# Kernel tuning notes

Hardware: AMD Instinct MI355X
Metric: run time of the kernel (lower is better)

Reference implementation:

```python
import jax, jax.numpy as jnp
import numpy as np

T, D = 10240, 64          # rows of base tensor, head dim (orig: 5, 4)
L = T // 5                # ragged split unit (orig split offsets 2/5 and 1/5)
SCALE = 1.0 / np.sqrt(D).astype(np.float32)


def setup_inputs() -> dict:
    key = jax.random.key(0)
    base_tensor = jax.random.normal(key, (T, D), dtype=jnp.float32)
    return {"base_tensor": base_tensor}


def _sdpa(q, k, v):
    # single-head SDPA over one ragged segment: q:(Sq,D) k,v:(Skv,D)
    scores = jnp.einsum('qd,kd->qk', q, k) * SCALE
    probs = jax.nn.softmax(scores, axis=-1)
    return jnp.einsum('qk,kd->qd', probs, v)


def reference(base_tensor):
    t1 = base_tensor                      # (T, D), orig view(5,4)
    t2 = t1 * 10.0
    # query path is detached in the original (clone().detach().requires_grad_())
    t1q = jax.lax.stop_gradient(t1)
    # ragged segments: q = [t1[:2L], t1[2L:]], kv = [t2[:L], t2[L:]]
    out0 = _sdpa(t1q[: 2 * L], t2[:L], t2[:L])
    out1 = _sdpa(t1q[2 * L :], t2[L:], t2[L:])
    loss = out0.sum() + out1.sum()        # sum over nested tensor values
    return loss
```

## Files before the change

kernel.cpp:

```cpp
#include <hip/hip_runtime.h>
#include <math.h>


#define T_ROWS 10240
#define SCALE2   1.80336880f
#define INV_S2   0.55451774f
#define SKIP_THR 35.0f

typedef __bf16 bf16x8 __attribute__((ext_vector_type(8)));
typedef float  f32x16 __attribute__((ext_vector_type(16)));
typedef float  f32x4v __attribute__((ext_vector_type(4)));

__device__ __forceinline__ float ex2(float x) {
    return __builtin_amdgcn_exp2f(x);
}

__device__ __forceinline__ float max16(const f32x16& a) {
    float h0 = fmaxf(fmaxf(a[0],  a[1]),  fmaxf(a[2],  a[3]));
    float h1 = fmaxf(fmaxf(a[4],  a[5]),  fmaxf(a[6],  a[7]));
    float h2 = fmaxf(fmaxf(a[8],  a[9]),  fmaxf(a[10], a[11]));
    float h3 = fmaxf(fmaxf(a[12], a[13]), fmaxf(a[14], a[15]));
    return fmaxf(fmaxf(h0, h1), fmaxf(h2, h3));
}

__global__ __launch_bounds__(256)
void prep_kernel(const float* __restrict__ base, __bf16* __restrict__ khi,
                 __bf16* __restrict__ klo, float* __restrict__ w,
                 float* __restrict__ selfs, float* __restrict__ Znm,
                 float* __restrict__ out) {
    int tid = threadIdx.x;
    if (blockIdx.x == 0 && tid == 0) *out = 0.f;
    if (tid < 64) Znm[blockIdx.x * 64 + tid] = 0.f;

    int row = blockIdx.x * 32 + (tid >> 3);
    int c0  = (tid & 7) << 3;
    const float* p = base + (size_t)row * 64 + c0;
    f32x4v a = *(const f32x4v*)p;
    f32x4v b = *(const f32x4v*)(p + 4);

    float sum = ((a[0] + a[1]) + (a[2] + a[3])) + ((b[0] + b[1]) + (b[2] + b[3]));
    float sq = a[0] * a[0];
    sq = fmaf(a[1], a[1], sq); sq = fmaf(a[2], a[2], sq); sq = fmaf(a[3], a[3], sq);
    sq = fmaf(b[0], b[0], sq); sq = fmaf(b[1], b[1], sq);
    sq = fmaf(b[2], b[2], sq); sq = fmaf(b[3], b[3], sq);
    #pragma unroll
    for (int off = 1; off < 8; off <<= 1) {
        sum += __shfl_xor(sum, off);
        sq  += __shfl_xor(sq, off);
    }
    if ((tid & 7) == 0) { w[row] = 10.0f * sum; selfs[row] = SCALE2 * sq; }

    bf16x8 h, l;
    #pragma unroll
    for (int j = 0; j < 4; ++j) {
        __bf16 h0 = (__bf16)a[j];
        h[j] = h0; l[j] = (__bf16)(a[j] - (float)h0);
        __bf16 h1 = (__bf16)b[j];
        h[j + 4] = h1; l[j + 4] = (__bf16)(b[j] - (float)h1);
    }
    int kt = row >> 5, lr = row & 31;
    int st = c0 >> 4, lh = (c0 >> 3) & 1;
    size_t dst = (size_t)kt * 2048 + st * 512 + lh * 256 + lr * 8;
    *(bf16x8*)(khi + dst) = h;
    *(bf16x8*)(klo + dst) = l;
}

__global__ __launch_bounds__(256, 4)
void attn_kernel(const __bf16* __restrict__ khi, const __bf16* __restrict__ klo,
                 const float* __restrict__ w, const float* __restrict__ selfs,
                 float* __restrict__ Znm) {
    const int lane  = threadIdx.x & 63;
    const int l31   = lane & 31;
    const int lhalf = lane >> 5;
    const int wv    = blockIdx.x * 4 + (threadIdx.x >> 6);

    if (wv < 384) {
        int qb, kt0; bool use_self;
        if (wv < 32)       { qb = wv * 64;                kt0 = (wv >> 2) * 8;          use_self = true;  }
        else if (wv < 288) { int i = wv - 32; qb = 2048 + (i >> 3) * 64; kt0 = (i & 7) * 8; use_self = false; }
        else               { int j = wv - 288; qb = 4096 + j * 64; kt0 = 64 + (8 + (j >> 2)) * 8; use_self = true; }

        #pragma unroll 1
        for (int s = 0; s < 2; ++s) {
            const int rb = (qb >> 5) + s;
            const __bf16* qp  = khi + (size_t)rb * 2048 + lane * 8;
            const __bf16* qlp = klo + (size_t)rb * 2048 + lane * 8;
            bf16x8 qh[4], ql[4];
            #pragma unroll
            for (int st = 0; st < 4; ++st) {
                qh[st] = *(const bf16x8*)(qp  + st * 512);
                ql[st] = *(const bf16x8*)(qlp + st * 512);
            }
            const int qrow = qb + s * 32 + l31;
            const float mref = use_self ? selfs[qrow] : 0.f;
            float z0 = 0.f, z1 = 0.f, z2 = 0.f, z3 = 0.f;
            float n0 = 0.f, n1 = 0.f, n2 = 0.f, n3 = 0.f;

            #pragma unroll 1
            for (int t = 0; t < 8; ++t) {
                f32x16 p, c;
                #pragma unroll
                for (int r = 0; r < 16; ++r) { p[r] = 0.f; c[r] = 0.f; }
                {
                    const __bf16* kp = khi + (size_t)(kt0 + t) * 2048 + lane * 8;
                    bf16x8 kh[4];
                    #pragma unroll
                    for (int st = 0; st < 4; ++st)
                        kh[st] = *(const bf16x8*)(kp + st * 512);
                    #pragma unroll
                    for (int st = 0; st < 4; ++st)
                        p = __builtin_amdgcn_mfma_f32_32x32x16_bf16(kh[st], qh[st], p, 0, 0, 0);
                    #pragma unroll
                    for (int st = 0; st < 4; ++st)
                        c = __builtin_amdgcn_mfma_f32_32x32x16_bf16(kh[st], ql[st], c, 0, 0, 0);
                }
                {
                    const __bf16* klp = klo + (size_t)(kt0 + t) * 2048 + lane * 8;
                    bf16x8 kl[4];
                    #pragma unroll
                    for (int st = 0; st < 4; ++st)
                        kl[st] = *(const bf16x8*)(klp + st * 512);
                    #pragma unroll
                    for (int st = 0; st < 4; ++st)
                        c = __builtin_amdgcn_mfma_f32_32x32x16_bf16(kl[st], qh[st], c, 0, 0, 0);
                }
                const float* wp = w + (kt0 + t) * 32 + lhalf * 4;
                #pragma unroll
                for (int g = 0; g < 4; ++g) {
                    f32x4v wv4 = *(const f32x4v*)(wp + g * 8);
                    float e0 = ex2(fmaf(c[g*4],   SCALE2, fmaf(p[g*4],   SCALE2, -mref)));
                    float e1 = ex2(fmaf(c[g*4+1], SCALE2, fmaf(p[g*4+1], SCALE2, -mref)));
                    float e2 = ex2(fmaf(c[g*4+2], SCALE2, fmaf(p[g*4+2], SCALE2, -mref)));
                    float e3 = ex2(fmaf(c[g*4+3], SCALE2, fmaf(p[g*4+3], SCALE2, -mref)));
                    z0 += e0; z1 += e1; z2 += e2; z3 += e3;
                    n0 = fmaf(e0, wv4[0], n0);
                    n1 = fmaf(e1, wv4[1], n1);
                    n2 = fmaf(e2, wv4[2], n2);
                    n3 = fmaf(e3, wv4[3], n3);
                }
            }
            float Z = (z0 + z1) + (z2 + z3);
            float N = (n0 + n1) + (n2 + n3);
            Z += __shfl(Z, lane ^ 32);
            N += __shfl(N, lane ^ 32);
            if (lhalf == 0) {
                atomicAdd(&Znm[2 * qrow],     Z);
                atomicAdd(&Znm[2 * qrow + 1], N);
            }
        }
    } else {
        int idx = wv - 384, qb, kt0;
        if (idx < 224) {
            int qw = idx / 7, cp = idx % 7, cd = qw >> 2;
            int c = cp + (cp >= cd);
            qb = qw * 64; kt0 = c * 8;
        } else {
            int i = idx - 224;
            int qw = i / 31, cp = i % 31, cd = 8 + (qw >> 2);
            int c = cp + (cp >= cd);
            qb = 4096 + qw * 64; kt0 = 64 + c * 8;
        }

        const int rb = qb >> 5;
        bf16x8 qh0[4], qh1[4];
        {
            const __bf16* q0 = khi + (size_t)rb * 2048 + lane * 8;
            #pragma unroll
            for (int st = 0; st < 4; ++st) {
                qh0[st] = *(const bf16x8*)(q0 + st * 512);
                qh1[st] = *(const bf16x8*)(q0 + 2048 + st * 512);
            }
        }
        const int qr0 = qb + l31, qr1 = qb + 32 + l31;
        const float mr0 = selfs[qr0], mr1 = selfs[qr1];
        const float th0 = (mr0 - SKIP_THR) * INV_S2;
        const float th1 = (mr1 - SKIP_THR) * INV_S2;
        float Z0 = 0.f, N0 = 0.f, Z1 = 0.f, N1 = 0.f;

        auto cold = [&](float& Zr, float& Nr, const bf16x8 (&qhs)[4],
                        int rbs, float mref, int t,
                        const f32x16& p, const bf16x8 (&kh)[4]) {
            f32x16 c = p;
            {
                const __bf16* qlp = klo + (size_t)rbs * 2048 + lane * 8;
                bf16x8 ql[4];
                #pragma unroll
                for (int st = 0; st < 4; ++st)
                    ql[st] = *(const bf16x8*)(qlp + st * 512);
                #pragma unroll
                for (int st = 0; st < 4; ++st)
                    c = __builtin_amdgcn_mfma_f32_32x32x16_bf16(kh[st], ql[st], c, 0, 0, 0);
            }
            {
                const __bf16* klp = klo + (size_t)(kt0 + t) * 2048 + lane * 8;
                bf16x8 kl[4];
                #pragma unroll
                for (int st = 0; st < 4; ++st)
                    kl[st] = *(const bf16x8*)(klp + st * 512);
                #pragma unroll
                for (int st = 0; st < 4; ++st)
                    c = __builtin_amdgcn_mfma_f32_32x32x16_bf16(kl[st], qhs[st], c, 0, 0, 0);
            }
            const float* wp = w + (kt0 + t) * 32 + lhalf * 4;
            float z0 = 0.f, z1 = 0.f, z2 = 0.f, z3 = 0.f;
            float n0 = 0.f, n1 = 0.f, n2 = 0.f, n3 = 0.f;
            #pragma unroll
            for (int g = 0; g < 4; ++g) {
                f32x4v wv4 = *(const f32x4v*)(wp + g * 8);
                float e0 = ex2(fmaf(c[g*4],   SCALE2, -mref));
                float e1 = ex2(fmaf(c[g*4+1], SCALE2, -mref));
                float e2 = ex2(fmaf(c[g*4+2], SCALE2, -mref));
                float e3 = ex2(fmaf(c[g*4+3], SCALE2, -mref));
                z0 += e0; z1 += e1; z2 += e2; z3 += e3;
                n0 = fmaf(e0, wv4[0], n0);
                n1 = fmaf(e1, wv4[1], n1);
                n2 = fmaf(e2, wv4[2], n2);
                n3 = fmaf(e3, wv4[3], n3);
            }
            Zr += (z0 + z1) + (z2 + z3);
            Nr += (n0 + n1) + (n2 + n3);
        };

        bf16x8 kb0[4], kb1[4];
        {
            const __bf16* kp = khi + (size_t)kt0 * 2048 + lane * 8;
            #pragma unroll
            for (int st = 0; st < 4; ++st) {
                kb0[st] = *(const bf16x8*)(kp + st * 512);
                kb1[st] = *(const bf16x8*)(kp + 2048 + st * 512);
            }
        }

        #pragma unroll 1
        for (int t = 0; t < 8; t += 2) {
            {
                f32x16 p0;
                #pragma unroll
                for (int r = 0; r < 16; ++r) p0[r] = 0.f;
                #pragma unroll
                for (int st = 0; st < 4; ++st)
                    p0 = __builtin_amdgcn_mfma_f32_32x32x16_bf16(kb0[st], qh0[st], p0, 0, 0, 0);
                if (!__all(max16(p0) <= th0)) cold(Z0, N0, qh0, rb,     mr0, t, p0, kb0);
                f32x16 p1;
                #pragma unroll
                for (int r = 0; r < 16; ++r) p1[r] = 0.f;
                #pragma unroll
                for (int st = 0; st < 4; ++st)
                    p1 = __builtin_amdgcn_mfma_f32_32x32x16_bf16(kb0[st], qh1[st], p1, 0, 0, 0);
                if (!__all(max16(p1) <= th1)) cold(Z1, N1, qh1, rb + 1, mr1, t, p1, kb0);
                int pf = (t + 2 < 8) ? t + 2 : t;
                const __bf16* kp = khi + (size_t)(kt0 + pf) * 2048 + lane * 8;
                #pragma unroll
                for (int st = 0; st < 4; ++st)
                    kb0[st] = *(const bf16x8*)(kp + st * 512);
            }
            {
                f32x16 p0;
                #pragma unroll
                for (int r = 0; r < 16; ++r) p0[r] = 0.f;
                #pragma unroll
                for (int st = 0; st < 4; ++st)
                    p0 = __builtin_amdgcn_mfma_f32_32x32x16_bf16(kb1[st], qh0[st], p0, 0, 0, 0);
                if (!__all(max16(p0) <= th0)) cold(Z0, N0, qh0, rb,     mr0, t + 1, p0, kb1);
                f32x16 p1;
                #pragma unroll
                for (int r = 0; r < 16; ++r) p1[r] = 0.f;
                #pragma unroll
                for (int st = 0; st < 4; ++st)
                    p1 = __builtin_amdgcn_mfma_f32_32x32x16_bf16(kb1[st], qh1[st], p1, 0, 0, 0);
                if (!__all(max16(p1) <= th1)) cold(Z1, N1, qh1, rb + 1, mr1, t + 1, p1, kb1);
                int pf = (t + 3 < 8) ? t + 3 : t + 1;
                const __bf16* kp = khi + (size_t)(kt0 + pf) * 2048 + lane * 8;
                #pragma unroll
                for (int st = 0; st < 4; ++st)
                    kb1[st] = *(const bf16x8*)(kp + st * 512);
            }
        }

        Z0 += __shfl(Z0, lane ^ 32); N0 += __shfl(N0, lane ^ 32);
        Z1 += __shfl(Z1, lane ^ 32); N1 += __shfl(N1, lane ^ 32);
        if (lhalf == 0) {
            atomicAdd(&Znm[2 * qr0],     Z0);
            atomicAdd(&Znm[2 * qr0 + 1], N0);
            atomicAdd(&Znm[2 * qr1],     Z1);
            atomicAdd(&Znm[2 * qr1 + 1], N1);
        }
    }
}

__global__ void reduce_kernel(const float* __restrict__ Znm,
                              float* __restrict__ out) {
    __shared__ float red[256];
    int gq = blockIdx.x * 256 + threadIdx.x;
    float contrib = Znm[2 * gq + 1] / Znm[2 * gq];
    red[threadIdx.x] = contrib;
    __syncthreads();
    #pragma unroll
    for (int s = 128; s > 0; s >>= 1) {
        if (threadIdx.x < s) red[threadIdx.x] += red[threadIdx.x + s];
        __syncthreads();
    }
    if (threadIdx.x == 0) atomicAdd(out, red[0]);
}

extern "C" void kernel_launch(void* const* d_in, const int* in_sizes, int n_in,
                              void* d_out, int out_size, void* d_ws, size_t ws_size,
                              hipStream_t stream) {
    const float* base = (const float*)d_in[0];
    float* out = (float*)d_out;
    float* ws  = (float*)d_ws;

    float*  w     = ws;
    float*  selfs = ws + T_ROWS;
    float*  Znm   = ws + 2 * T_ROWS;
    __bf16* khi   = (__bf16*)(ws + 4 * T_ROWS);
    __bf16* klo   = khi + 320 * 2048;

    prep_kernel<<<T_ROWS / 32, 256, 0, stream>>>(base, khi, klo, w, selfs, Znm, out);
    attn_kernel<<<896, 256, 0, stream>>>(khi, klo, w, selfs, Znm);
    reduce_kernel<<<T_ROWS / 256, 256, 0, stream>>>(Znm, out);
}
```

Before: 29.64 us.

## Defer skipped-tile exact recompute into bitmask replay pass and raise MFMA priority

The skip-screening loop now only records, in per-row-group bitmasks, which key tiles exceed the threshold, instead of branching into the exact computation inline. After the screening pass, a replay loop recomputes only the flagged tiles, reloading the hi and lo key parts and redoing the full hi*hi product. The aim is a tight, branch-free screening loop with better MFMA issue and prefetching. s_setprio hints are also placed around the MFMA bursts. The cost is extra reloads and an extra hi*hi MFMA pass for every flagged tile.

```diff
diff --git a/kernel.cpp b/kernel.cpp
--- a/kernel.cpp
+++ b/kernel.cpp
@@ -107,12 +107,14 @@
                     #pragma unroll
                     for (int st = 0; st < 4; ++st)
                         kh[st] = *(const bf16x8*)(kp + st * 512);
+                    __builtin_amdgcn_s_setprio(1);
                     #pragma unroll
                     for (int st = 0; st < 4; ++st)
                         p = __builtin_amdgcn_mfma_f32_32x32x16_bf16(kh[st], qh[st], p, 0, 0, 0);
                     #pragma unroll
                     for (int st = 0; st < 4; ++st)
                         c = __builtin_amdgcn_mfma_f32_32x32x16_bf16(kh[st], ql[st], c, 0, 0, 0);
+                    __builtin_amdgcn_s_setprio(0);
                 }
                 {
                     const __bf16* klp = klo + (size_t)(kt0 + t) * 2048 + lane * 8;
@@ -120,9 +122,11 @@
                     #pragma unroll
                     for (int st = 0; st < 4; ++st)
                         kl[st] = *(const bf16x8*)(klp + st * 512);
+                    __builtin_amdgcn_s_setprio(1);
                     #pragma unroll
                     for (int st = 0; st < 4; ++st)
                         c = __builtin_amdgcn_mfma_f32_32x32x16_bf16(kl[st], qh[st], c, 0, 0, 0);
+                    __builtin_amdgcn_s_setprio(0);
                 }
                 const float* wp = w + (kt0 + t) * 32 + lhalf * 4;
                 #pragma unroll
@@ -175,51 +179,8 @@
         const float mr0 = selfs[qr0], mr1 = selfs[qr1];
         const float th0 = (mr0 - SKIP_THR) * INV_S2;
         const float th1 = (mr1 - SKIP_THR) * INV_S2;
-        float Z0 = 0.f, N0 = 0.f, Z1 = 0.f, N1 = 0.f;
-
-        auto cold = [&](float& Zr, float& Nr, const bf16x8 (&qhs)[4],
-                        int rbs, float mref, int t,
-                        const f32x16& p, const bf16x8 (&kh)[4]) {
-            f32x16 c = p;
-            {
-                const __bf16* qlp = klo + (size_t)rbs * 2048 + lane * 8;
-                bf16x8 ql[4];
-                #pragma unroll
-                for (int st = 0; st < 4; ++st)
-                    ql[st] = *(const bf16x8*)(qlp + st * 512);
-                #pragma unroll
-                for (int st = 0; st < 4; ++st)
-                    c = __builtin_amdgcn_mfma_f32_32x32x16_bf16(kh[st], ql[st], c, 0, 0, 0);
-            }
-            {
-                const __bf16* klp = klo + (size_t)(kt0 + t) * 2048 + lane * 8;
-                bf16x8 kl[4];
-                #pragma unroll
-                for (int st = 0; st < 4; ++st)
-                    kl[st] = *(const bf16x8*)(klp + st * 512);
-                #pragma unroll
-                for (int st = 0; st < 4; ++st)
-                    c = __builtin_amdgcn_mfma_f32_32x32x16_bf16(kl[st], qhs[st], c, 0, 0, 0);
-            }
-            const float* wp = w + (kt0 + t) * 32 + lhalf * 4;
-            float z0 = 0.f, z1 = 0.f, z2 = 0.f, z3 = 0.f;
-            float n0 = 0.f, n1 = 0.f, n2 = 0.f, n3 = 0.f;
-            #pragma unroll
-            for (int g = 0; g < 4; ++g) {
-                f32x4v wv4 = *(const f32x4v*)(wp + g * 8);
-                float e0 = ex2(fmaf(c[g*4],   SCALE2, -mref));
-                float e1 = ex2(fmaf(c[g*4+1], SCALE2, -mref));
-                float e2 = ex2(fmaf(c[g*4+2], SCALE2, -mref));
-                float e3 = ex2(fmaf(c[g*4+3], SCALE2, -mref));
-                z0 += e0; z1 += e1; z2 += e2; z3 += e3;
-                n0 = fmaf(e0, wv4[0], n0);
-                n1 = fmaf(e1, wv4[1], n1);
-                n2 = fmaf(e2, wv4[2], n2);
-                n3 = fmaf(e3, wv4[3], n3);
-            }
-            Zr += (z0 + z1) + (z2 + z3);
-            Nr += (n0 + n1) + (n2 + n3);
-        };
+
+        unsigned smask0 = 0, smask1 = 0;
 
         bf16x8 kb0[4], kb1[4];
         {
@@ -234,20 +195,19 @@
         #pragma unroll 1
         for (int t = 0; t < 8; t += 2) {
             {
-                f32x16 p0;
-                #pragma unroll
-                for (int r = 0; r < 16; ++r) p0[r] = 0.f;
+                f32x16 p0, p1;
+                #pragma unroll
+                for (int r = 0; r < 16; ++r) { p0[r] = 0.f; p1[r] = 0.f; }
+                __builtin_amdgcn_s_setprio(1);
                 #pragma unroll
                 for (int st = 0; st < 4; ++st)
                     p0 = __builtin_amdgcn_mfma_f32_32x32x16_bf16(kb0[st], qh0[st], p0, 0, 0, 0);
-                if (!__all(max16(p0) <= th0)) cold(Z0, N0, qh0, rb,     mr0, t, p0, kb0);
-                f32x16 p1;
-                #pragma unroll
-                for (int r = 0; r < 16; ++r) p1[r] = 0.f;
                 #pragma unroll
                 for (int st = 0; st < 4; ++st)
                     p1 = __builtin_amdgcn_mfma_f32_32x32x16_bf16(kb0[st], qh1[st], p1, 0, 0, 0);
-                if (!__all(max16(p1) <= th1)) cold(Z1, N1, qh1, rb + 1, mr1, t, p1, kb0);
+                __builtin_amdgcn_s_setprio(0);
+                smask0 |= (!__all(max16(p0) <= th0)) ? (1u << t) : 0u;
+                smask1 |= (!__all(max16(p1) <= th1)) ? (1u << t) : 0u;
                 int pf = (t + 2 < 8) ? t + 2 : t;
                 const __bf16* kp = khi + (size_t)(kt0 + pf) * 2048 + lane * 8;
                 #pragma unroll
@@ -255,20 +215,19 @@
                     kb0[st] = *(const bf16x8*)(kp + st * 512);
             }
             {
-                f32x16 p0;
-                #pragma unroll
-                for (int r = 0; r < 16; ++r) p0[r] = 0.f;
+                f32x16 p0, p1;
+                #pragma unroll
+                for (int r = 0; r < 16; ++r) { p0[r] = 0.f; p1[r] = 0.f; }
+                __builtin_amdgcn_s_setprio(1);
                 #pragma unroll
                 for (int st = 0; st < 4; ++st)
                     p0 = __builtin_amdgcn_mfma_f32_32x32x16_bf16(kb1[st], qh0[st], p0, 0, 0, 0);
-                if (!__all(max16(p0) <= th0)) cold(Z0, N0, qh0, rb,     mr0, t + 1, p0, kb1);
-                f32x16 p1;
-                #pragma unroll
-                for (int r = 0; r < 16; ++r) p1[r] = 0.f;
                 #pragma unroll
                 for (int st = 0; st < 4; ++st)
                     p1 = __builtin_amdgcn_mfma_f32_32x32x16_bf16(kb1[st], qh1[st], p1, 0, 0, 0);
-                if (!__all(max16(p1) <= th1)) cold(Z1, N1, qh1, rb + 1, mr1, t + 1, p1, kb1);
+                __builtin_amdgcn_s_setprio(0);
+                smask0 |= (!__all(max16(p0) <= th0)) ? (1u << (t + 1)) : 0u;
+                smask1 |= (!__all(max16(p1) <= th1)) ? (1u << (t + 1)) : 0u;
                 int pf = (t + 3 < 8) ? t + 3 : t + 1;
                 const __bf16* kp = khi + (size_t)(kt0 + pf) * 2048 + lane * 8;
                 #pragma unroll
@@ -276,6 +235,65 @@
                     kb1[st] = *(const bf16x8*)(kp + st * 512);
             }
         }
+
+        float Z0 = 0.f, N0 = 0.f, Z1 = 0.f, N1 = 0.f;
+        auto replay = [&](unsigned m, const bf16x8 (&qhs)[4], int rbs,
+                          float mref, float& Zr, float& Nr) {
+            while (m) {
+                int t = __builtin_ctz(m); m &= m - 1;
+                f32x16 c;
+                #pragma unroll
+                for (int r = 0; r < 16; ++r) c[r] = 0.f;
+                {
+                    const __bf16* kp = khi + (size_t)(kt0 + t) * 2048 + lane * 8;
+                    bf16x8 kh[4];
+                    #pragma unroll
+                    for (int st = 0; st < 4; ++st)
+                        kh[st] = *(const bf16x8*)(kp + st * 512);
+                    #pragma unroll
+                    for (int st = 0; st < 4; ++st)
+                        c = __builtin_amdgcn_mfma_f32_32x32x16_bf16(kh[st], qhs[st], c, 0, 0, 0);
+                    const __bf16* qlp = klo + (size_t)rbs * 2048 + lane * 8;
+                    bf16x8 ql[4];
+                    #pragma unroll
+                    for (int st = 0; st < 4; ++st)
+                        ql[st] = *(const bf16x8*)(qlp + st * 512);
+                    #pragma unroll
+                    for (int st = 0; st < 4; ++st)
+                        c = __builtin_amdgcn_mfma_f32_32x32x16_bf16(kh[st], ql[st], c, 0, 0, 0);
+                }
+                {
+                    const __bf16* klp = klo + (size_t)(kt0 + t) * 2048 + lane * 8;
+                    bf16x8 kl[4];
+                    #pragma unroll
+                    for (int st = 0; st < 4; ++st)
+                        kl[st] = *(const bf16x8*)(klp + st * 512);
+                    #pragma unroll
+                    for (int st = 0; st < 4; ++st)
+                        c = __builtin_amdgcn_mfma_f32_32x32x16_bf16(kl[st], qhs[st], c, 0, 0, 0);
+                }
+                const float* wp = w + (kt0 + t) * 32 + lhalf * 4;
+                float z0 = 0.f, z1 = 0.f, z2 = 0.f, z3 = 0.f;
+                float n0 = 0.f, n1 = 0.f, n2 = 0.f, n3 = 0.f;
+                #pragma unroll
+                for (int g = 0; g < 4; ++g) {
+                    f32x4v wv4 = *(const f32x4v*)(wp + g * 8);
+                    float e0 = ex2(fmaf(c[g*4],   SCALE2, -mref));
+                    float e1 = ex2(fmaf(c[g*4+1], SCALE2, -mref));
+                    float e2 = ex2(fmaf(c[g*4+2], SCALE2, -mref));
+                    float e3 = ex2(fmaf(c[g*4+3], SCALE2, -mref));
+                    z0 += e0; z1 += e1; z2 += e2; z3 += e3;
+                    n0 = fmaf(e0, wv4[0], n0);
+                    n1 = fmaf(e1, wv4[1], n1);
+                    n2 = fmaf(e2, wv4[2], n2);
+                    n3 = fmaf(e3, wv4[3], n3);
+                }
+                Zr += (z0 + z1) + (z2 + z3);
+                Nr += (n0 + n1) + (n2 + n3);
+            }
+        };
+        replay(smask0, qh0, rb,     mr0, Z0, N0);
+        replay(smask1, qh1, rb + 1, mr1, Z1, N1);
 
         Z0 += __shfl(Z0, lane ^ 32); N0 += __shfl(N0, lane ^ 32);
         Z1 += __shfl(Z1, lane ^ 32); N1 += __shfl(N1, lane ^ 32);
```

Measured after the change: 30.55 us. +3.1%, slower.
